# Kernel optimization log

Hardware: AMD Instinct MI355X
Metric: run time of the kernel (lower is better)

## Reference

```python
import jax, jax.numpy as jnp
import numpy as np

K = 8               # config.k
X_MIN = -1.0        # x_min
X_MAX = 1.0         # x_max
GLOBAL_COEFF = 1.0  # config.global_coeff
EPS = 1e-8          # torch cosine_similarity eps
BZ, P, D = 8192, 1024, 1024  # batch, num_pool, data_dim


def setup_inputs() -> dict:
    key = jax.random.key(0)
    k1, k2, k3, k4, k5 = jax.random.split(key, 5)
    return {
        "ppg": jax.random.normal(k1, (BZ, 1, D), dtype=jnp.float32),
        "keys_pool": jax.random.normal(k2, (P, D), dtype=jnp.float32),
        "prompt_pool": jax.random.normal(k3, (P, D), dtype=jnp.float32),
        "cnn_w": jax.random.normal(k4, (1, 1, 3), dtype=jnp.float32) * 0.5,
        "cnn_b": jax.random.normal(k5, (1,), dtype=jnp.float32) * 0.1,
    }


def _prompt_cnn(prompt, w, b):
    # PromptCNN: Conv1d(1,1,k=3,pad=1) + ReLU on [P, D]
    x = prompt[:, None, :]  # [P, 1, D]
    y = jax.lax.conv_general_dilated(
        x, w, window_strides=(1,), padding=((1, 1),),
        dimension_numbers=("NCH", "OIH", "NCH"))
    y = jax.nn.relu(y + b[None, :, None])
    return y[:, 0, :]  # [P, D]


def _global_normalizer(prompt, x_min, x_max):
    pmax = jnp.max(prompt, axis=-1, keepdims=True)
    pmin = jnp.min(prompt, axis=-1, keepdims=True)
    scale = (x_max - x_min) / (pmax - pmin)
    return scale * (prompt - pmin) + x_min


def reference(ppg, keys_pool, prompt_pool, cnn_w, cnn_b):
    # prompt pool through CNN
    pcnn = _prompt_cnn(prompt_pool, cnn_w, cnn_b)  # [P, D]

    # cosine similarity: ppg [bz,1,D] vs keys [P,D] -> [bz,P]
    pn = ppg[:, 0, :] / jnp.maximum(
        jnp.linalg.norm(ppg[:, 0, :], axis=-1, keepdims=True), EPS)
    kn = keys_pool / jnp.maximum(
        jnp.linalg.norm(keys_pool, axis=-1, keepdims=True), EPS)
    cos = jnp.einsum("bd,pd->bp", pn, kn)  # [bz, P]
    score_ = 1.0 - cos

    # top-k smallest distances (largest=False) -> ascending order
    neg_vals, idx = jax.lax.top_k(-score_, K)  # [bz, K]
    score = -neg_vals

    # entropy of softmax over raw scores
    logp = jax.nn.log_softmax(score_, axis=-1)
    entropy = -(jnp.exp(logp) * logp).sum(axis=-1).mean()

    # gather selected prompts, average over k, add singleton channel dim
    prompt = pcnn[idx].mean(axis=1)[:, None, :]  # [bz, 1, D]

    # min-max global normalization (glonorm=True)
    prompt = _global_normalizer(prompt, X_MIN, X_MAX)

    # additive combine (mul=False)
    prompted = ppg + GLOBAL_COEFF * prompt  # [bz, 1, D]

    return prompted, score.mean(), entropy
```

## Files before the change

kernel.cpp:

```cpp
#include <hip/hip_runtime.h>
#include <hip/hip_bf16.h>

#define BZ 8192
#define PP 1024
#define DD 1024
#define KSEL 8

typedef unsigned short u16;
typedef __attribute__((ext_vector_type(8))) short bf16x8;
typedef __attribute__((ext_vector_type(4))) float f32x4;

#define WS_INVK 0
#define WS_INVP 1024
#define WS_SCORE 9216
#define WS_ENT 17408
#define WS_IDX 25600
#define WS_BF16_BYTE 368640ull

__device__ __forceinline__ u16 f2bf(float x) {
  __hip_bfloat16 h = __float2bfloat16(x);
  return *(u16*)&h;
}
__device__ __forceinline__ float bf2f(u16 u) {
  __hip_bfloat16 h; *(u16*)&h = u;
  return __bfloat162float(h);
}
__device__ __forceinline__ void gll16(const void* g, void* l) {
  __builtin_amdgcn_global_load_lds((__attribute__((address_space(1))) void*)g,
                                   (__attribute__((address_space(3))) void*)l, 16, 0, 0);
}

__global__ __launch_bounds__(256) void convert_kernel(const float* __restrict__ ppg,
                                                      const float* __restrict__ keys,
                                                      float* __restrict__ ws) {
  u16* Ahi = (u16*)((char*)ws + WS_BF16_BYTE);
  u16* Alo = Ahi + 8388608;
  u16* Bhi = Alo + 8388608;
  u16* Blo = Bhi + 1048576;

  int blk = blockIdx.x;
  const float* src; u16 *hi, *lo; float* invdst;
  if (blk < PP) {
    src = keys + (size_t)blk * DD;
    hi = Bhi + (size_t)blk * DD; lo = Blo + (size_t)blk * DD;
    invdst = ws + WS_INVK + blk;
  } else {
    int r = blk - PP;
    src = ppg + (size_t)r * DD;
    hi = Ahi + (size_t)r * DD; lo = Alo + (size_t)r * DD;
    invdst = ws + WS_INVP + r;
  }
  int t = threadIdx.x;
  float4 v = ((const float4*)src)[t];
  float x[4] = {v.x, v.y, v.z, v.w};
  u16 h4[4], l4[4];
  float s = 0.f;
  #pragma unroll
  for (int j = 0; j < 4; ++j) {
    h4[j] = f2bf(x[j]);
    l4[j] = f2bf(x[j] - bf2f(h4[j]));
    s += x[j] * x[j];
  }
  *(ushort4*)(hi + t * 4) = *(ushort4*)h4;
  *(ushort4*)(lo + t * 4) = *(ushort4*)l4;

  __shared__ float red[4];
  #pragma unroll
  for (int o = 32; o > 0; o >>= 1) s += __shfl_down(s, o);
  if ((t & 63) == 0) red[t >> 6] = s;
  __syncthreads();
  if (t == 0) {
    float tot = red[0] + red[1] + red[2] + red[3];
    *invdst = 1.0f / fmaxf(sqrtf(tot), 1e-8f);
  }
}

#define LDS_AH 0
#define LDS_AL 8192
#define LDS_BH 16384
#define LDS_BL 24576

__global__ __launch_bounds__(256, 2) void gemm_mfma(const float* __restrict__ ws_ro,
                                                    float* __restrict__ C) {
  const u16* Ahi = (const u16*)((const char*)ws_ro + WS_BF16_BYTE);
  const u16* Alo = Ahi + 8388608;
  const u16* Bhi = Alo + 8388608;
  const u16* Blo = Bhi + 1048576;

  __shared__ u16 lds[32768];

  int t = threadIdx.x;
  int wid = t >> 6, lane = t & 63;
  int lr = lane & 15, lg = lane >> 4;

  int orig = blockIdx.x;
  int wg = (orig & 7) * 64 + (orig >> 3);
  int bm0 = (wg >> 3) * 128;
  int bn0 = (wg & 7) * 128;
  int wm = wid >> 1, wn = wid & 1;

  size_t offA[4], offB[4];
  int ldso[4];
  #pragma unroll
  for (int r = 0; r < 4; ++r) {
    int s = r * 256 + t;
    int row = s >> 3, g = s & 7;
    offA[r] = (size_t)(bm0 + row) * DD + g * 8;
    offB[r] = (size_t)(bn0 + row) * DD + g * 8;
    ldso[r] = (r * 256 + wid * 64) * 8;
  }

  f32x4 acc[4][4] = {};

  for (int kt = 0; kt < 16; ++kt) {
    int k0 = kt * 64;
    #pragma unroll
    for (int r = 0; r < 4; ++r) {
      gll16(Ahi + offA[r] + k0, &lds[LDS_AH + ldso[r]]);
      gll16(Alo + offA[r] + k0, &lds[LDS_AL + ldso[r]]);
      gll16(Bhi + offB[r] + k0, &lds[LDS_BH + ldso[r]]);
      gll16(Blo + offB[r] + k0, &lds[LDS_BL + ldso[r]]);
    }
    __syncthreads();

    #pragma unroll
    for (int kh = 0; kh < 2; ++kh) {
      bf16x8 ah[4], al[4], bh[4], bl[4];
      #pragma unroll
      for (int i = 0; i < 4; ++i) {
        int off = (wm * 64 + i * 16 + lr) * 64 + kh * 32 + lg * 8;
        ah[i] = *(const bf16x8*)&lds[LDS_AH + off];
        al[i] = *(const bf16x8*)&lds[LDS_AL + off];
      }
      #pragma unroll
      for (int j = 0; j < 4; ++j) {
        int off = (wn * 64 + j * 16 + lr) * 64 + kh * 32 + lg * 8;
        bh[j] = *(const bf16x8*)&lds[LDS_BH + off];
        bl[j] = *(const bf16x8*)&lds[LDS_BL + off];
      }
      #pragma unroll
      for (int i = 0; i < 4; ++i)
        #pragma unroll
        for (int j = 0; j < 4; ++j) {
          acc[i][j] = __builtin_amdgcn_mfma_f32_16x16x32_bf16(ah[i], bh[j], acc[i][j], 0, 0, 0);
          acc[i][j] = __builtin_amdgcn_mfma_f32_16x16x32_bf16(ah[i], bl[j], acc[i][j], 0, 0, 0);
          acc[i][j] = __builtin_amdgcn_mfma_f32_16x16x32_bf16(al[i], bh[j], acc[i][j], 0, 0, 0);
        }
    }
    __syncthreads();
  }

  const float* invP = ws_ro + WS_INVP;
  const float* invK = ws_ro + WS_INVK;
  #pragma unroll
  for (int i = 0; i < 4; ++i) {
    #pragma unroll
    for (int q = 0; q < 4; ++q) {
      int row = bm0 + wm * 64 + i * 16 + lg * 4 + q;
      float ip = invP[row];
      #pragma unroll
      for (int j = 0; j < 4; ++j) {
        int col = bn0 + wn * 64 + j * 16 + lr;
        C[(size_t)row * PP + col] = acc[i][j][q] * ip * invK[col];
      }
    }
  }
}

__global__ __launch_bounds__(256) void topk_wave_kernel(const float* __restrict__ cosm,
                                                        float* __restrict__ ws) {
  int wid = threadIdx.x >> 6, lane = threadIdx.x & 63;
  int row = blockIdx.x * 4 + wid;
  const float* crow = cosm + (size_t)row * PP;

  float c[16];
  #pragma unroll
  for (int p = 0; p < 4; ++p) {
    f32x4 v = *(const f32x4*)(crow + p * 256 + lane * 4);
    c[p * 4 + 0] = v[0]; c[p * 4 + 1] = v[1]; c[p * 4 + 2] = v[2]; c[p * 4 + 3] = v[3];
  }

  float z = 0.f, w = 0.f;
  #pragma unroll
  for (int l = 0; l < 16; ++l) {
    float s = 1.0f - c[l];
    float e = __expf(s - 2.0f);
    z += e; w += s * e;
  }
  #pragma unroll
  for (int o = 1; o < 64; o <<= 1) { z += __shfl_xor(z, o); w += __shfl_xor(w, o); }
  if (lane == 0) ws[WS_ENT + row] = 2.0f + __logf(z) - w / z;

  unsigned used = 0;
  float score_sum = 0.f;
  int myidx = 0;
  #pragma unroll
  for (int it = 0; it < KSEL; ++it) {
    float v = -2.0f; int gi = 1 << 30;
    #pragma unroll
    for (int l = 0; l < 16; ++l) {
      if (!((used >> l) & 1u)) {
        float cv = c[l];
        int g = ((l >> 2) << 8) | (lane << 2) | (l & 3);
        if (cv > v || (cv == v && g < gi)) { v = cv; gi = g; }
      }
    }
    #pragma unroll
    for (int o = 1; o < 64; o <<= 1) {
      float ov = __shfl_xor(v, o);
      int og = __shfl_xor(gi, o);
      if (ov > v || (ov == v && og < gi)) { v = ov; gi = og; }
    }
    score_sum += 1.0f - v;
    if (((gi >> 2) & 63) == lane) used |= 1u << ((((gi >> 8) & 3) << 2) | (gi & 3));
    if (lane == it) myidx = gi;
  }
  if (lane == 0) ws[WS_SCORE + row] = score_sum;
  if (lane < KSEL) ((int*)(ws + WS_IDX))[row * KSEL + lane] = myidx;
}

__global__ __launch_bounds__(256) void prompt_kernel(const float* __restrict__ ppg,
                                                     const float* __restrict__ pool,
                                                     const float* __restrict__ cw,
                                                     const float* __restrict__ cb,
                                                     const float* __restrict__ ws,
                                                     float* __restrict__ out) {
  int row = blockIdx.x;
  int t = threadIdx.x;
  int lane = t & 63;
  const int* idx = (const int*)(ws + WS_IDX) + row * KSEL;
  float w0 = cw[0], w1 = cw[1], w2 = cw[2], bb = cb[0];
  int d0 = t * 4;

  float a0 = 0.f, a1 = 0.f, a2 = 0.f, a3 = 0.f;
  #pragma unroll
  for (int j = 0; j < KSEL; ++j) {
    int r = idx[j];
    const float* src = pool + (size_t)r * DD;
    f32x4 x = *(const f32x4*)(src + d0);
    float xm_n = __shfl_up(x[3], 1);
    float xp_n = __shfl_down(x[0], 1);
    float xm, xp;
    if (lane == 0)       xm = (t > 0)   ? src[d0 - 1] : 0.f;
    else                 xm = xm_n;
    if (lane == 63)      xp = (t < 255) ? src[d0 + 4] : 0.f;
    else                 xp = xp_n;
    float y0 = fmaf(w0, xm,   fmaf(w1, x[0], fmaf(w2, x[1], bb)));
    float y1 = fmaf(w0, x[0], fmaf(w1, x[1], fmaf(w2, x[2], bb)));
    float y2 = fmaf(w0, x[1], fmaf(w1, x[2], fmaf(w2, x[3], bb)));
    float y3 = fmaf(w0, x[2], fmaf(w1, x[3], fmaf(w2, xp,   bb)));
    a0 += fmaxf(y0, 0.f);
    a1 += fmaxf(y1, 0.f);
    a2 += fmaxf(y2, 0.f);
    a3 += fmaxf(y3, 0.f);
  }
  a0 *= 0.125f; a1 *= 0.125f; a2 *= 0.125f; a3 *= 0.125f;

  __shared__ float rmin[4], rmax[4];
  float lmin = fminf(fminf(a0, a1), fminf(a2, a3));
  float lmax = fmaxf(fmaxf(a0, a1), fmaxf(a2, a3));
  #pragma unroll
  for (int o = 32; o > 0; o >>= 1) {
    lmin = fminf(lmin, __shfl_down(lmin, o));
    lmax = fmaxf(lmax, __shfl_down(lmax, o));
  }
  if ((t & 63) == 0) { rmin[t >> 6] = lmin; rmax[t >> 6] = lmax; }
  __syncthreads();
  float pmin = fminf(fminf(rmin[0], rmin[1]), fminf(rmin[2], rmin[3]));
  float pmax = fmaxf(fmaxf(rmax[0], rmax[1]), fmaxf(rmax[2], rmax[3]));
  float scale = 2.0f / (pmax - pmin);

  f32x4 pv = *(const f32x4*)(ppg + (size_t)row * DD + d0);
  f32x4 o4;
  o4[0] = pv[0] + (scale * (a0 - pmin) - 1.0f);
  o4[1] = pv[1] + (scale * (a1 - pmin) - 1.0f);
  o4[2] = pv[2] + (scale * (a2 - pmin) - 1.0f);
  o4[3] = pv[3] + (scale * (a3 - pmin) - 1.0f);
  *(f32x4*)(out + (size_t)row * DD + d0) = o4;
}

__global__ __launch_bounds__(256) void finalize_kernel(const float* __restrict__ ws,
                                                       float* __restrict__ out) {
  int t = threadIdx.x;
  const float* ss = ws + WS_SCORE;
  const float* ee = ws + WS_ENT;
  float s = 0.f, e = 0.f;
  for (int i = t; i < BZ; i += 256) { s += ss[i]; e += ee[i]; }
  __shared__ float rs[4], re[4];
  #pragma unroll
  for (int o = 32; o > 0; o >>= 1) { s += __shfl_down(s, o); e += __shfl_down(e, o); }
  if ((t & 63) == 0) { rs[t >> 6] = s; re[t >> 6] = e; }
  __syncthreads();
  if (t == 0) {
    float sT = rs[0] + rs[1] + rs[2] + rs[3];
    float eT = re[0] + re[1] + re[2] + re[3];
    out[(size_t)BZ * DD + 0] = sT / (float)(BZ * KSEL);
    out[(size_t)BZ * DD + 1] = eT / (float)BZ;
  }
}

extern "C" void kernel_launch(void* const* d_in, const int* in_sizes, int n_in,
                              void* d_out, int out_size, void* d_ws, size_t ws_size,
                              hipStream_t stream) {
  const float* ppg  = (const float*)d_in[0];
  const float* keys = (const float*)d_in[1];
  const float* pool = (const float*)d_in[2];
  const float* cw   = (const float*)d_in[3];
  const float* cb   = (const float*)d_in[4];
  float* out = (float*)d_out;
  float* ws  = (float*)d_ws;

  hipLaunchKernelGGL(convert_kernel, dim3(PP + BZ), dim3(256), 0, stream, ppg, keys, ws);
  hipLaunchKernelGGL(gemm_mfma, dim3((BZ / 128) * (PP / 128)), dim3(256), 0, stream, ws, out);
  hipLaunchKernelGGL(topk_wave_kernel, dim3(BZ / 4), dim3(256), 0, stream, out, ws);
  hipLaunchKernelGGL(prompt_kernel, dim3(BZ), dim3(256), 0, stream, ppg, pool, cw, cb, ws, out);
  hipLaunchKernelGGL(finalize_kernel, dim3(1), dim3(256), 0, stream, ws, out);
}
```

Baseline: 135.6 us.

## Fuse partial top-k and softmax stats into GEMM epilogue, merge in prompt kernel

The GEMM epilogue now computes per-row, per-64-column-slice softmax partial sums (z, w) and a local top-8 with indices, instead of writing the full cosine matrix. The prompt kernel merges the 16 slice candidates per row into the final top-8, reduces the entropy partials, then runs the gather/CNN/normalise step. This removes the full 8192x1024 fp32 write and read-back and drops one kernel launch. In exchange the GEMM epilogue gains 8 shuffle-based selection rounds, which adds register pressure, and the merge is serialised in one wave before a block barrier.

```diff
diff --git a/kernel.cpp b/kernel.cpp
--- a/kernel.cpp
+++ b/kernel.cpp
@@ -14,8 +14,8 @@
 #define WS_INVP 1024
 #define WS_SCORE 9216
 #define WS_ENT 17408
-#define WS_IDX 25600
 #define WS_BF16_BYTE 368640ull
+#define WS_ZW_BYTE 38117376ull
 
 __device__ __forceinline__ u16 f2bf(float x) {
   __hip_bfloat16 h = __float2bfloat16(x);
@@ -80,9 +80,9 @@
 #define LDS_BH 16384
 #define LDS_BL 24576
 
-__global__ __launch_bounds__(256, 2) void gemm_mfma(const float* __restrict__ ws_ro,
+__global__ __launch_bounds__(256, 2) void gemm_mfma(float* __restrict__ ws,
                                                     float* __restrict__ C) {
-  const u16* Ahi = (const u16*)((const char*)ws_ro + WS_BF16_BYTE);
+  const u16* Ahi = (const u16*)((const char*)ws + WS_BF16_BYTE);
   const u16* Alo = Ahi + 8388608;
   const u16* Bhi = Alo + 8388608;
   const u16* Blo = Bhi + 1048576;
@@ -150,101 +150,141 @@
     __syncthreads();
   }
 
-  const float* invP = ws_ro + WS_INVP;
-  const float* invK = ws_ro + WS_INVK;
+  const float* invP = ws + WS_INVP;
+  const float* invK = ws + WS_INVK;
+  float* zw = (float*)((char*)ws + WS_ZW_BYTE);
+  int slice = ((wg & 7) << 1) | wn;
+
+  float ik[4];
+  int gcol[4];
+  #pragma unroll
+  for (int j = 0; j < 4; ++j) {
+    gcol[j] = bn0 + wn * 64 + j * 16 + lr;
+    ik[j] = invK[gcol[j]];
+  }
+
   #pragma unroll
   for (int i = 0; i < 4; ++i) {
     #pragma unroll
     for (int q = 0; q < 4; ++q) {
       int row = bm0 + wm * 64 + i * 16 + lg * 4 + q;
       float ip = invP[row];
+      float val[4];
+      #pragma unroll
+      for (int j = 0; j < 4; ++j) val[j] = acc[i][j][q] * ip * ik[j];
+
+      float z = 0.f, w = 0.f;
       #pragma unroll
       for (int j = 0; j < 4; ++j) {
-        int col = bn0 + wn * 64 + j * 16 + lr;
-        C[(size_t)row * PP + col] = acc[i][j][q] * ip * invK[col];
-      }
-    }
-  }
-}
-
-__global__ __launch_bounds__(256) void topk_wave_kernel(const float* __restrict__ cosm,
-                                                        float* __restrict__ ws) {
-  int wid = threadIdx.x >> 6, lane = threadIdx.x & 63;
-  int row = blockIdx.x * 4 + wid;
-  const float* crow = cosm + (size_t)row * PP;
-
-  float c[16];
-  #pragma unroll
-  for (int p = 0; p < 4; ++p) {
-    f32x4 v = *(const f32x4*)(crow + p * 256 + lane * 4);
-    c[p * 4 + 0] = v[0]; c[p * 4 + 1] = v[1]; c[p * 4 + 2] = v[2]; c[p * 4 + 3] = v[3];
-  }
-
-  float z = 0.f, w = 0.f;
-  #pragma unroll
-  for (int l = 0; l < 16; ++l) {
-    float s = 1.0f - c[l];
-    float e = __expf(s - 2.0f);
-    z += e; w += s * e;
-  }
-  #pragma unroll
-  for (int o = 1; o < 64; o <<= 1) { z += __shfl_xor(z, o); w += __shfl_xor(w, o); }
-  if (lane == 0) ws[WS_ENT + row] = 2.0f + __logf(z) - w / z;
-
-  unsigned used = 0;
-  float score_sum = 0.f;
-  int myidx = 0;
-  #pragma unroll
-  for (int it = 0; it < KSEL; ++it) {
-    float v = -2.0f; int gi = 1 << 30;
-    #pragma unroll
-    for (int l = 0; l < 16; ++l) {
-      if (!((used >> l) & 1u)) {
-        float cv = c[l];
-        int g = ((l >> 2) << 8) | (lane << 2) | (l & 3);
-        if (cv > v || (cv == v && g < gi)) { v = cv; gi = g; }
-      }
-    }
-    #pragma unroll
-    for (int o = 1; o < 64; o <<= 1) {
-      float ov = __shfl_xor(v, o);
-      int og = __shfl_xor(gi, o);
-      if (ov > v || (ov == v && og < gi)) { v = ov; gi = og; }
-    }
-    score_sum += 1.0f - v;
-    if (((gi >> 2) & 63) == lane) used |= 1u << ((((gi >> 8) & 3) << 2) | (gi & 3));
-    if (lane == it) myidx = gi;
-  }
-  if (lane == 0) ws[WS_SCORE + row] = score_sum;
-  if (lane < KSEL) ((int*)(ws + WS_IDX))[row * KSEL + lane] = myidx;
-}
-
-__global__ __launch_bounds__(256) void prompt_kernel(const float* __restrict__ ppg,
-                                                     const float* __restrict__ pool,
-                                                     const float* __restrict__ cw,
-                                                     const float* __restrict__ cb,
-                                                     const float* __restrict__ ws,
-                                                     float* __restrict__ out) {
+        float s = 1.0f - val[j];
+        float e = __expf(s - 2.0f);
+        z += e; w += s * e;
+      }
+      #pragma unroll
+      for (int o = 1; o < 16; o <<= 1) { z += __shfl_xor(z, o); w += __shfl_xor(w, o); }
+      if (lr == 0) {
+        zw[((size_t)row * 16 + slice) * 2 + 0] = z;
+        zw[((size_t)row * 16 + slice) * 2 + 1] = w;
+      }
+
+      float wv = -2.0f; int wgi = 0;
+      #pragma unroll
+      for (int it = 0; it < KSEL; ++it) {
+        float v = -2.0f; int gi = 1 << 30;
+        #pragma unroll
+        for (int j = 0; j < 4; ++j) {
+          if (val[j] > v || (val[j] == v && gcol[j] < gi)) { v = val[j]; gi = gcol[j]; }
+        }
+        #pragma unroll
+        for (int o = 1; o < 16; o <<= 1) {
+          float ov = __shfl_xor(v, o);
+          int og = __shfl_xor(gi, o);
+          if (ov > v || (ov == v && og < gi)) { v = ov; gi = og; }
+        }
+        if (lr == it) { wv = v; wgi = gi; }
+        #pragma unroll
+        for (int j = 0; j < 4; ++j) if (gcol[j] == gi) val[j] = -2.0f;
+      }
+      if (lr < KSEL) {
+        C[(size_t)row * 1024 + slice * 16 + lr] = wv;
+        ((int*)C)[(size_t)row * 1024 + slice * 16 + 8 + lr] = wgi;
+      }
+    }
+  }
+}
+
+__global__ __launch_bounds__(256) void prompt_merge_kernel(
+    const float* __restrict__ ppg, const float* __restrict__ pool,
+    const float* __restrict__ cw, const float* __restrict__ cb,
+    float* __restrict__ ws, float* __restrict__ out) {
   int row = blockIdx.x;
   int t = threadIdx.x;
   int lane = t & 63;
-  const int* idx = (const int*)(ws + WS_IDX) + row * KSEL;
+
+  __shared__ int sel[KSEL];
+  __shared__ float rmin[4], rmax[4];
+
+  if (t < 64) {
+    const float* crow_f = out + (size_t)row * 1024;
+    const int* crow_i = (const int*)crow_f;
+    float cval[2]; int cg[2];
+    #pragma unroll
+    for (int e = 0; e < 2; ++e) {
+      int c = lane + e * 64;
+      cval[e] = crow_f[(c >> 3) * 16 + (c & 7)];
+      cg[e] = crow_i[(c >> 3) * 16 + 8 + (c & 7)];
+    }
+    float ssum = 0.f;
+    int myidx = 0;
+    #pragma unroll
+    for (int it = 0; it < KSEL; ++it) {
+      float v = -2.0f; int gi = 1 << 30;
+      #pragma unroll
+      for (int e = 0; e < 2; ++e) {
+        if (cval[e] > v || (cval[e] == v && cg[e] < gi)) { v = cval[e]; gi = cg[e]; }
+      }
+      #pragma unroll
+      for (int o = 1; o < 64; o <<= 1) {
+        float ov = __shfl_xor(v, o);
+        int og = __shfl_xor(gi, o);
+        if (ov > v || (ov == v && og < gi)) { v = ov; gi = og; }
+      }
+      ssum += 1.0f - v;
+      if (lane == it) myidx = gi;
+      #pragma unroll
+      for (int e = 0; e < 2; ++e) if (cg[e] == gi) cval[e] = -2.0f;
+    }
+    if (lane == 0) ws[WS_SCORE + row] = ssum;
+    if (lane < KSEL) sel[lane] = myidx;
+
+    const float* zw = (const float*)((const char*)ws + WS_ZW_BYTE);
+    float z = 0.f, w = 0.f;
+    if (lane < 16) {
+      z = zw[((size_t)row * 16 + lane) * 2 + 0];
+      w = zw[((size_t)row * 16 + lane) * 2 + 1];
+    }
+    #pragma unroll
+    for (int o = 1; o < 64; o <<= 1) { z += __shfl_xor(z, o); w += __shfl_xor(w, o); }
+    if (lane == 0) ws[WS_ENT + row] = 2.0f + __logf(z) - w / z;
+  }
+  __syncthreads();
+
   float w0 = cw[0], w1 = cw[1], w2 = cw[2], bb = cb[0];
   int d0 = t * 4;
 
   float a0 = 0.f, a1 = 0.f, a2 = 0.f, a3 = 0.f;
   #pragma unroll
   for (int j = 0; j < KSEL; ++j) {
-    int r = idx[j];
+    int r = sel[j];
     const float* src = pool + (size_t)r * DD;
     f32x4 x = *(const f32x4*)(src + d0);
     float xm_n = __shfl_up(x[3], 1);
     float xp_n = __shfl_down(x[0], 1);
     float xm, xp;
-    if (lane == 0)       xm = (t > 0)   ? src[d0 - 1] : 0.f;
-    else                 xm = xm_n;
-    if (lane == 63)      xp = (t < 255) ? src[d0 + 4] : 0.f;
-    else                 xp = xp_n;
+    if (lane == 0)  xm = (t > 0)   ? src[d0 - 1] : 0.f;
+    else            xm = xm_n;
+    if (lane == 63) xp = (t < 255) ? src[d0 + 4] : 0.f;
+    else            xp = xp_n;
     float y0 = fmaf(w0, xm,   fmaf(w1, x[0], fmaf(w2, x[1], bb)));
     float y1 = fmaf(w0, x[0], fmaf(w1, x[1], fmaf(w2, x[2], bb)));
     float y2 = fmaf(w0, x[1], fmaf(w1, x[2], fmaf(w2, x[3], bb)));
@@ -256,7 +296,6 @@
   }
   a0 *= 0.125f; a1 *= 0.125f; a2 *= 0.125f; a3 *= 0.125f;
 
-  __shared__ float rmin[4], rmax[4];
   float lmin = fminf(fminf(a0, a1), fminf(a2, a3));
   float lmax = fmaxf(fmaxf(a0, a1), fmaxf(a2, a3));
   #pragma unroll
@@ -312,7 +351,7 @@
 
   hipLaunchKernelGGL(convert_kernel, dim3(PP + BZ), dim3(256), 0, stream, ppg, keys, ws);
   hipLaunchKernelGGL(gemm_mfma, dim3((BZ / 128) * (PP / 128)), dim3(256), 0, stream, ws, out);
-  hipLaunchKernelGGL(topk_wave_kernel, dim3(BZ / 4), dim3(256), 0, stream, out, ws);
-  hipLaunchKernelGGL(prompt_kernel, dim3(BZ), dim3(256), 0, stream, ppg, pool, cw, cb, ws, out);
+  hipLaunchKernelGGL(prompt_merge_kernel, dim3(BZ), dim3(256), 0, stream,
+                     ppg, pool, cw, cb, ws, out);
   hipLaunchKernelGGL(finalize_kernel, dim3(1), dim3(256), 0, stream, ws, out);
 }
```

Result: slower. 352.9 us (+160.2%).

## Fuse top-k selection into the prompt gather/normalize kernel

Applied to the files above, without the earlier changes.

Merges the separate top-k/entropy kernel into the prompt kernel. Wave 0 of each block reads the cosine row, computes the entropy terms and the top-8 indices, and writes the indices to shared memory; the whole block then gathers, convolves and normalizes the selected prompts. This removes one kernel launch and the global round trip for the indices. In exchange, three of the four waves in each block sit idle during selection. It also relies on the cosine row being read before the same row of the output buffer is overwritten.

```diff
diff --git a/kernel.cpp b/kernel.cpp
--- a/kernel.cpp
+++ b/kernel.cpp
@@ -14,7 +14,6 @@
 #define WS_INVP 1024
 #define WS_SCORE 9216
 #define WS_ENT 17408
-#define WS_IDX 25600
 #define WS_BF16_BYTE 368640ull
 
 __device__ __forceinline__ u16 f2bf(float x) {
@@ -167,84 +166,80 @@
   }
 }
 
-__global__ __launch_bounds__(256) void topk_wave_kernel(const float* __restrict__ cosm,
-                                                        float* __restrict__ ws) {
-  int wid = threadIdx.x >> 6, lane = threadIdx.x & 63;
-  int row = blockIdx.x * 4 + wid;
-  const float* crow = cosm + (size_t)row * PP;
-
-  float c[16];
-  #pragma unroll
-  for (int p = 0; p < 4; ++p) {
-    f32x4 v = *(const f32x4*)(crow + p * 256 + lane * 4);
-    c[p * 4 + 0] = v[0]; c[p * 4 + 1] = v[1]; c[p * 4 + 2] = v[2]; c[p * 4 + 3] = v[3];
-  }
-
-  float z = 0.f, w = 0.f;
-  #pragma unroll
-  for (int l = 0; l < 16; ++l) {
-    float s = 1.0f - c[l];
-    float e = __expf(s - 2.0f);
-    z += e; w += s * e;
-  }
-  #pragma unroll
-  for (int o = 1; o < 64; o <<= 1) { z += __shfl_xor(z, o); w += __shfl_xor(w, o); }
-  if (lane == 0) ws[WS_ENT + row] = 2.0f + __logf(z) - w / z;
-
-  unsigned used = 0;
-  float score_sum = 0.f;
-  int myidx = 0;
-  #pragma unroll
-  for (int it = 0; it < KSEL; ++it) {
-    float v = -2.0f; int gi = 1 << 30;
-    #pragma unroll
-    for (int l = 0; l < 16; ++l) {
-      if (!((used >> l) & 1u)) {
-        float cv = c[l];
-        int g = ((l >> 2) << 8) | (lane << 2) | (l & 3);
-        if (cv > v || (cv == v && g < gi)) { v = cv; gi = g; }
-      }
-    }
-    #pragma unroll
-    for (int o = 1; o < 64; o <<= 1) {
-      float ov = __shfl_xor(v, o);
-      int og = __shfl_xor(gi, o);
-      if (ov > v || (ov == v && og < gi)) { v = ov; gi = og; }
-    }
-    score_sum += 1.0f - v;
-    if (((gi >> 2) & 63) == lane) used |= 1u << ((((gi >> 8) & 3) << 2) | (gi & 3));
-    if (lane == it) myidx = gi;
-  }
-  if (lane == 0) ws[WS_SCORE + row] = score_sum;
-  if (lane < KSEL) ((int*)(ws + WS_IDX))[row * KSEL + lane] = myidx;
-}
-
-__global__ __launch_bounds__(256) void prompt_kernel(const float* __restrict__ ppg,
-                                                     const float* __restrict__ pool,
-                                                     const float* __restrict__ cw,
-                                                     const float* __restrict__ cb,
-                                                     const float* __restrict__ ws,
-                                                     float* __restrict__ out) {
+__global__ __launch_bounds__(256) void fused_topk_prompt(
+    const float* __restrict__ ppg, const float* __restrict__ pool,
+    const float* __restrict__ cw, const float* __restrict__ cb,
+    float* __restrict__ ws, float* __restrict__ out) {
   int row = blockIdx.x;
   int t = threadIdx.x;
-  int lane = t & 63;
-  const int* idx = (const int*)(ws + WS_IDX) + row * KSEL;
+  int w = t >> 6, lane = t & 63;
+
+  __shared__ int sel[KSEL];
+  __shared__ float rmin[4], rmax[4];
+
+  if (w == 0) {
+    const float* crow = out + (size_t)row * PP;
+    float c[16];
+    #pragma unroll
+    for (int p = 0; p < 4; ++p) {
+      f32x4 v = *(const f32x4*)(crow + p * 256 + lane * 4);
+      c[p * 4 + 0] = v[0]; c[p * 4 + 1] = v[1]; c[p * 4 + 2] = v[2]; c[p * 4 + 3] = v[3];
+    }
+
+    float z = 0.f, wv = 0.f;
+    #pragma unroll
+    for (int l = 0; l < 16; ++l) {
+      float s = 1.0f - c[l];
+      float e = __expf(s - 2.0f);
+      z += e; wv += s * e;
+    }
+    #pragma unroll
+    for (int o = 1; o < 64; o <<= 1) { z += __shfl_xor(z, o); wv += __shfl_xor(wv, o); }
+    if (lane == 0) ws[WS_ENT + row] = 2.0f + __logf(z) - wv / z;
+
+    unsigned used = 0;
+    float score_sum = 0.f;
+    #pragma unroll
+    for (int it = 0; it < KSEL; ++it) {
+      float v = -2.0f; int gi = 1 << 30;
+      #pragma unroll
+      for (int l = 0; l < 16; ++l) {
+        if (!((used >> l) & 1u)) {
+          float cv = c[l];
+          int g = ((l >> 2) << 8) | (lane << 2) | (l & 3);
+          if (cv > v || (cv == v && g < gi)) { v = cv; gi = g; }
+        }
+      }
+      #pragma unroll
+      for (int o = 1; o < 64; o <<= 1) {
+        float ov = __shfl_xor(v, o);
+        int og = __shfl_xor(gi, o);
+        if (ov > v || (ov == v && og < gi)) { v = ov; gi = og; }
+      }
+      score_sum += 1.0f - v;
+      if (((gi >> 2) & 63) == lane) used |= 1u << ((((gi >> 8) & 3) << 2) | (gi & 3));
+      if (lane == it) sel[it] = gi;
+    }
+    if (lane == 0) ws[WS_SCORE + row] = score_sum;
+  }
+  __syncthreads();
+
   float w0 = cw[0], w1 = cw[1], w2 = cw[2], bb = cb[0];
   int d0 = t * 4;
 
   float a0 = 0.f, a1 = 0.f, a2 = 0.f, a3 = 0.f;
   #pragma unroll
   for (int j = 0; j < KSEL; ++j) {
-    int r = idx[j];
+    int r = sel[j];
     const float* src = pool + (size_t)r * DD;
     f32x4 x = *(const f32x4*)(src + d0);
     float xm_n = __shfl_up(x[3], 1);
     float xp_n = __shfl_down(x[0], 1);
     float xm, xp;
-    if (lane == 0)       xm = (t > 0)   ? src[d0 - 1] : 0.f;
-    else                 xm = xm_n;
-    if (lane == 63)      xp = (t < 255) ? src[d0 + 4] : 0.f;
-    else                 xp = xp_n;
+    if (lane == 0)  xm = (t > 0)   ? src[d0 - 1] : 0.f;
+    else            xm = xm_n;
+    if (lane == 63) xp = (t < 255) ? src[d0 + 4] : 0.f;
+    else            xp = xp_n;
     float y0 = fmaf(w0, xm,   fmaf(w1, x[0], fmaf(w2, x[1], bb)));
     float y1 = fmaf(w0, x[0], fmaf(w1, x[1], fmaf(w2, x[2], bb)));
     float y2 = fmaf(w0, x[1], fmaf(w1, x[2], fmaf(w2, x[3], bb)));
@@ -256,7 +251,6 @@
   }
   a0 *= 0.125f; a1 *= 0.125f; a2 *= 0.125f; a3 *= 0.125f;
 
-  __shared__ float rmin[4], rmax[4];
   float lmin = fminf(fminf(a0, a1), fminf(a2, a3));
   float lmax = fmaxf(fmaxf(a0, a1), fmaxf(a2, a3));
   #pragma unroll
@@ -312,7 +306,7 @@
 
   hipLaunchKernelGGL(convert_kernel, dim3(PP + BZ), dim3(256), 0, stream, ppg, keys, ws);
   hipLaunchKernelGGL(gemm_mfma, dim3((BZ / 128) * (PP / 128)), dim3(256), 0, stream, ws, out);
-  hipLaunchKernelGGL(topk_wave_kernel, dim3(BZ / 4), dim3(256), 0, stream, out, ws);
-  hipLaunchKernelGGL(prompt_kernel, dim3(BZ), dim3(256), 0, stream, ppg, pool, cw, cb, ws, out);
+  hipLaunchKernelGGL(fused_topk_prompt, dim3(BZ), dim3(256), 0, stream,
+                     ppg, pool, cw, cb, ws, out);
   hipLaunchKernelGGL(finalize_kernel, dim3(1), dim3(256), 0, stream, ws, out);
 }
```

After: 154.0 us. 13.5% more time.
